# Performance work log

Measured on AMD Instinct MI355X. Metric: run time of the kernel, lower is better.

The kernel has to match this reference:

```python
import jax, jax.numpy as jnp
import numpy as np

B, S, D_IN, D_OUT = 4, 2048, 1024, 1024

def setup_inputs() -> dict:
    key = jax.random.key(0)
    k1, k2, k3, k4, k5, k6 = jax.random.split(key, 6)
    return {
        "inputs_for_keys": jax.random.normal(k1, (B, S, D_IN), dtype=jnp.float32),
        "inputs_for_values": jax.random.normal(k2, (B, S, D_IN), dtype=jnp.float32),
        "inputs_for_queries": jax.random.normal(k3, (B, S, D_IN), dtype=jnp.float32),
        "WK": jax.random.truncated_normal(k4, -2.0, 2.0, (D_IN, D_OUT), dtype=jnp.float32) * 0.1,
        "WV": jax.random.truncated_normal(k5, -2.0, 2.0, (D_IN, D_OUT), dtype=jnp.float32) * 0.1,
        "WQ": jax.random.truncated_normal(k6, -2.0, 2.0, (D_IN, D_OUT), dtype=jnp.float32) * 0.1,
    }

def reference(inputs_for_keys, inputs_for_values, inputs_for_queries, WK, WV, WQ):
    # projections: [B,S,D_in] @ [D_in,D_out] -> [B,S,D_out]
    K = jnp.einsum('bsd,de->bse', inputs_for_keys, WK)
    V = jnp.einsum('bsd,de->bse', inputs_for_values, WV)
    Q = jnp.einsum('bsd,de->bse', inputs_for_queries, WQ)
    # scores: [B,S,S]. NOTE: original TF code scales by sqrt(K.shape[1]) = sqrt(seq_len),
    # not sqrt(head_dim) — reproduce that faithfully.
    scale = jnp.sqrt(jnp.float32(K.shape[1]))
    scores = jnp.einsum('bqe,bke->bqk', Q, K) / scale
    attn = jax.nn.softmax(scores, axis=-1)
    return jnp.einsum('bqk,bke->bqe', attn, V)
```

## Files before the change

### kernel.cpp

```cpp
#include <hip/hip_runtime.h>
#include <hip/hip_bf16.h>


typedef __attribute__((ext_vector_type(4))) float    f32x4;
typedef __attribute__((ext_vector_type(8))) _Float16 f16x8;
typedef __attribute__((ext_vector_type(4))) _Float16 f16x4;

constexpr size_t MiB = 1u << 20;
constexpr size_t MK  = (size_t)8192 * 1024;
constexpr size_t WSZ = (size_t)1024 * 1024;

__device__ __forceinline__ void gload_lds16(const void* g, void* l) {
  __builtin_amdgcn_global_load_lds(
      (const __attribute__((address_space(1))) unsigned int*)g,
      (__attribute__((address_space(3))) unsigned int*)l, 16, 0, 0);
}

#define MFMA16(a, b, c) __builtin_amdgcn_mfma_f32_16x16x32_f16(a, b, c, 0, 0, 0)

__device__ __forceinline__ void swz_block(int& bx, int& by, int& bz) {
  unsigned gx = gridDim.x, gy = gridDim.y;
  unsigned flat = blockIdx.x + gx * (blockIdx.y + gy * blockIdx.z);
  unsigned total = gx * gy * gridDim.z;
  unsigned cpx = total >> 3;
  unsigned s = (flat & 7) * cpx + (flat >> 3);
  bx = s % gx; s /= gx; by = s % gy; bz = s / gy;
}

__global__ __launch_bounds__(256) void prep(
    const float* __restrict__ x0, const float* __restrict__ x1,
    const float* __restrict__ x2, _Float16* __restrict__ XF,
    const float* __restrict__ w0, const float* __restrict__ w1,
    const float* __restrict__ w2, _Float16* __restrict__ WT)
{
  const unsigned id = blockIdx.x;
  if (id < 24576) {
    const int z = id >> 13;
    const unsigned blk = id & 8191;
    const float* x = z == 0 ? x0 : (z == 1 ? x1 : x2);
    size_t i = ((size_t)blk * 256 + threadIdx.x) * 4;
    float4 v = *(const float4*)(x + i);
    f16x4 h = {(_Float16)v.x, (_Float16)v.y, (_Float16)v.z, (_Float16)v.w};
    *(f16x4*)(XF + (size_t)z * MK + i) = h;
  } else {
    const unsigned rem = id - 24576;
    const int z = rem >> 10;
    const unsigned blk = rem & 1023;
    const float* W = z == 0 ? w0 : (z == 1 ? w1 : w2);
    _Float16* o = WT + (size_t)z * WSZ;
    __shared__ float tile[32][33];
    const int bx = (blk & 31) * 32;
    const int by = (blk >> 5) * 32;
    const int tx = threadIdx.x & 31, ty = threadIdx.x >> 5;
    #pragma unroll
    for (int r = 0; r < 32; r += 8)
      tile[ty + r][tx] = W[(size_t)(by + ty + r) * 1024 + bx + tx];
    __syncthreads();
    #pragma unroll
    for (int r = 0; r < 32; r += 8)
      o[(size_t)(bx + ty + r) * 1024 + by + tx] = (_Float16)tile[tx][ty + r];
  }
}

template <int MODE>
__global__ __launch_bounds__(512, 4) void gemmO(
    const _Float16* __restrict__ At, size_t sAz, int lda,
    const _Float16* __restrict__ Bt, size_t sBz, int ldb,
    void* __restrict__ Cv, size_t sCz, int ldc,
    int K, float scale)
{
  extern __shared__ char lds[];
  int bx, by, bz;
  swz_block(bx, by, bz);
  const _Float16* A = At + (size_t)bz * sAz;
  const _Float16* B = Bt + (size_t)bz * sBz;

  const int gm0 = by * 256, gn0 = bx * 128;
  const int tid = threadIdx.x;
  const int lane = tid & 63, wave = tid >> 6;
  const int wm = (wave >> 1) * 64;
  const int wn = (wave & 1) * 64;
  const int fr = lane & 15, fq = lane >> 4;
  const int nkt = K >> 5;

  const int clog = ((tid & 3) ^ ((tid >> 3) & 3)) * 8;
  const _Float16* srcA = A + (size_t)(gm0 + (tid >> 2)) * lda + clog;
  const _Float16* srcB = B + (size_t)(gn0 + (tid >> 2)) * ldb + clog;
  char* const dst0 = lds + tid * 16;

  auto STG = [&](int tile) {
    const int off = tile * 32;
    char* d = dst0 + (tile % 3) * 24576;
    gload_lds16(srcA + off,                     d);
    gload_lds16(srcA + off + (size_t)128 * lda, d + 8192);
    gload_lds16(srcB + off,                     d + 16384);
  };

  const int pc  = (fq ^ ((fr >> 1) & 3)) * 16;
  const int arb = (wm + fr) * 64 + pc;
  const int brb = 16384 + (wn + fr) * 64 + pc;

  f32x4 acc[4][4] = {};
  f16x8 af[4], bfr[4];

  STG(0);
  if (nkt > 1) {
    STG(1);
    asm volatile("s_waitcnt vmcnt(3)" ::: "memory");
  } else {
    asm volatile("s_waitcnt vmcnt(0)" ::: "memory");
  }
  __builtin_amdgcn_s_barrier();
  __builtin_amdgcn_sched_barrier(0);

  for (int t = 0; t < nkt; ++t) {
    const char* buf = lds + (t % 3) * 24576;
    const bool st2 = (t + 2) < nkt;

    if (st2) STG(t + 2);

    #pragma unroll
    for (int mi = 0; mi < 4; ++mi)
      af[mi] = *(const f16x8*)(buf + arb + mi * 1024);
    #pragma unroll
    for (int ni = 0; ni < 4; ++ni)
      bfr[ni] = *(const f16x8*)(buf + brb + ni * 1024);

    __builtin_amdgcn_s_setprio(1);
    #pragma unroll
    for (int mi = 0; mi < 4; ++mi)
      #pragma unroll
      for (int ni = 0; ni < 4; ++ni)
        acc[mi][ni] = MFMA16(af[mi], bfr[ni], acc[mi][ni]);
    __builtin_amdgcn_s_setprio(0);

    if (st2)               asm volatile("s_waitcnt vmcnt(3)" ::: "memory");
    else if (t + 1 < nkt)  asm volatile("s_waitcnt vmcnt(0)" ::: "memory");
    __builtin_amdgcn_s_barrier();
    __builtin_amdgcn_sched_barrier(0);
  }

  const int erow = gm0 + wm + fq * 4;
  const int ecol = gn0 + wn + fr;
  #pragma unroll
  for (int m = 0; m < 4; ++m)
    #pragma unroll
    for (int n = 0; n < 4; ++n) {
      size_t base = (size_t)(erow + m * 16) * ldc + (ecol + n * 16);
      #pragma unroll
      for (int r = 0; r < 4; ++r) {
        float v = acc[m][n][r];
        size_t idx = base + (size_t)r * ldc;
        if constexpr (MODE == 0)
          ((float*)Cv + (size_t)bz * sCz)[idx] = v * scale;
        else if constexpr (MODE == 1)
          ((_Float16*)Cv + (size_t)bz * sCz)[idx] = (_Float16)v;
        else
          ((_Float16*)Cv + (size_t)bz * sCz)[idx] = (_Float16)(v * scale);
      }
    }
}

__global__ __launch_bounds__(256) void softmax_rows(
    const _Float16* __restrict__ S, _Float16* __restrict__ P)
{
  const int w = threadIdx.x >> 6, lane = threadIdx.x & 63;
  const size_t row = (size_t)blockIdx.x * 4 + w;
  const _Float16* sr = S + row * 2048;

  f16x8 v[4];
  #pragma unroll
  for (int c = 0; c < 4; ++c)
    v[c] = *(const f16x8*)(sr + c * 512 + lane * 8);

  float m = -1e30f;
  #pragma unroll
  for (int c = 0; c < 4; ++c)
    #pragma unroll
    for (int j = 0; j < 8; ++j) m = fmaxf(m, (float)v[c][j]);
  #pragma unroll
  for (int o = 32; o >= 1; o >>= 1) m = fmaxf(m, __shfl_xor(m, o));

  float e[4][8];
  float s = 0.f;
  #pragma unroll
  for (int c = 0; c < 4; ++c)
    #pragma unroll
    for (int j = 0; j < 8; ++j) {
      e[c][j] = __expf((float)v[c][j] - m);
      s += e[c][j];
    }
  #pragma unroll
  for (int o = 32; o >= 1; o >>= 1) s += __shfl_xor(s, o);

  const float inv = 1.0f / s;
  _Float16* pr = P + row * 2048;
  #pragma unroll
  for (int c = 0; c < 4; ++c) {
    f16x8 p;
    #pragma unroll
    for (int j = 0; j < 8; ++j) p[j] = (_Float16)(e[c][j] * inv);
    *(f16x8*)(pr + c * 512 + lane * 8) = p;
  }
}

extern "C" void kernel_launch(void* const* d_in, const int* in_sizes, int n_in,
                              void* d_out, int out_size, void* d_ws, size_t ws_size,
                              hipStream_t stream)
{
  const float* Xk = (const float*)d_in[0];
  const float* Xv = (const float*)d_in[1];
  const float* Xq = (const float*)d_in[2];
  const float* WK = (const float*)d_in[3];
  const float* WV = (const float*)d_in[4];
  const float* WQ = (const float*)d_in[5];
  float* out = (float*)d_out;
  char* ws = (char*)d_ws;

  _Float16* XF   = (_Float16*)(ws);
  _Float16* WT   = (_Float16*)(ws + 48 * MiB);
  _Float16* PROJ = (_Float16*)(ws + 54 * MiB);
  _Float16* VTf  = (_Float16*)(ws + 86 * MiB);
  _Float16* SC   = (_Float16*)(ws + 102 * MiB);
  _Float16* P    = (_Float16*)(ws);

  _Float16* Kp = PROJ;
  _Float16* Qp = PROJ + MK;

  auto* f1 = gemmO<1>;
  auto* f2 = gemmO<2>;
  auto* f0 = gemmO<0>;
  (void)hipFuncSetAttribute((const void*)f1, hipFuncAttributeMaxDynamicSharedMemorySize, 73728);
  (void)hipFuncSetAttribute((const void*)f2, hipFuncAttributeMaxDynamicSharedMemorySize, 73728);
  (void)hipFuncSetAttribute((const void*)f0, hipFuncAttributeMaxDynamicSharedMemorySize, 73728);

  prep<<<dim3(27648), 256, 0, stream>>>(Xk, Xv, Xq, XF, WK, WV, WQ, WT);
  gemmO<1><<<dim3(8, 32, 2), 512, 73728, stream>>>(
      XF, 2 * MK, 1024, WT, 2 * WSZ, 1024,
      PROJ, MK, 1024, 1024, 1.0f);
  gemmO<1><<<dim3(64, 4, 1), 512, 73728, stream>>>(
      WT + WSZ, 0, 1024, XF + MK, 0, 1024,
      VTf, 0, 8192, 1024, 1.0f);
  gemmO<2><<<dim3(16, 8, 4), 512, 73728, stream>>>(
      Qp, (size_t)2048 * 1024, 1024, Kp, (size_t)2048 * 1024, 1024,
      SC, (size_t)2048 * 2048, 2048, 1024, 0.022097086912079608f);
  softmax_rows<<<dim3(2048), 256, 0, stream>>>(SC, P);
  gemmO<0><<<dim3(8, 8, 4), 512, 73728, stream>>>(
      P, (size_t)2048 * 2048, 2048, VTf, 2048, 8192,
      out, (size_t)2048 * 1024, 1024, 2048, 1.0f);
}
```

Measured before the change: 195.3 us.

## Add 256x256 8-wave phased GEMM for K/Q projection and QK^T scores

Measured after the change: 183.0 us. -6.3%, faster.

```diff
diff --git a/kernel.cpp b/kernel.cpp
--- a/kernel.cpp
+++ b/kernel.cpp
@@ -34,16 +34,20 @@
     const float* __restrict__ w2, _Float16* __restrict__ WT)
 {
   const unsigned id = blockIdx.x;
-  if (id < 24576) {
-    const int z = id >> 13;
-    const unsigned blk = id & 8191;
-    const float* x = z == 0 ? x0 : (z == 1 ? x1 : x2);
-    size_t i = ((size_t)blk * 256 + threadIdx.x) * 4;
-    float4 v = *(const float4*)(x + i);
-    f16x4 h = {(_Float16)v.x, (_Float16)v.y, (_Float16)v.z, (_Float16)v.w};
-    *(f16x4*)(XF + (size_t)z * MK + i) = h;
+  if (id < 6144) {
+    const int z = id >> 11;
+    const unsigned blk = id & 2047;
+    const float* x = (z == 0 ? x0 : (z == 1 ? x1 : x2)) + (size_t)blk * 4096;
+    _Float16* o = XF + (size_t)z * MK + (size_t)blk * 4096;
+    #pragma unroll
+    for (int j = 0; j < 4; ++j) {
+      size_t i = (size_t)j * 1024 + threadIdx.x * 4;
+      float4 v = *(const float4*)(x + i);
+      f16x4 h = {(_Float16)v.x, (_Float16)v.y, (_Float16)v.z, (_Float16)v.w};
+      *(f16x4*)(o + i) = h;
+    }
   } else {
-    const unsigned rem = id - 24576;
+    const unsigned rem = id - 6144;
     const int z = rem >> 10;
     const unsigned blk = rem & 1023;
     const float* W = z == 0 ? w0 : (z == 1 ? w1 : w2);
@@ -60,6 +64,167 @@
     for (int r = 0; r < 32; r += 8)
       o[(size_t)(bx + ty + r) * 1024 + by + tx] = (_Float16)tile[tx][ty + r];
   }
+}
+
+template <int MODE>
+__global__ __launch_bounds__(512, 2) void gemm8p(
+    const _Float16* __restrict__ At, size_t sA,
+    const _Float16* __restrict__ Bt, size_t sB,
+    void* __restrict__ Cv, size_t sCz,
+    int N, int K, float scale)
+{
+  extern __shared__ char lds[];
+  int bx, by, bz;
+  swz_block(bx, by, bz);
+  const _Float16* A = At + (size_t)bz * sA;
+  const _Float16* B = Bt + (size_t)bz * sB;
+
+  const int gm0 = by * 256, gn0 = bx * 256;
+  const int tid = threadIdx.x;
+  const int lane = tid & 63, wave = tid >> 6;
+  const int wm = (wave >> 2) * 128;
+  const int wn = (wave & 3) * 64;
+  const int fr = lane & 15, fq = lane >> 4;
+  const int nkt = K >> 6;
+
+  const int clog = ((tid & 7) ^ ((tid >> 3) & 7)) * 8;
+  const _Float16* srcA = A + (size_t)(gm0 + (tid >> 3)) * K + clog;
+  const _Float16* srcB = B + (size_t)(gn0 + (tid >> 3)) * K + clog;
+  char* const dst0 = lds + tid * 16;
+
+  auto SH = [&](int tile, int h) {
+    const _Float16* s = (h < 2 ? srcA : srcB) + (size_t)((h & 1) * 128) * K
+                        + tile * 64;
+    char* d = dst0 + (tile & 1) * 65536 + h * 16384;
+    gload_lds16(s, d);
+    gload_lds16(s + (size_t)64 * K, d + 8192);
+  };
+
+  const int axor = fr & 7;
+  const int pc0 = (fq ^ axor) * 16;
+  const int pc1 = ((4 + fq) ^ axor) * 16;
+  const int arb = (wm + fr) * 128;
+  const int brb = 32768 + (wn + fr) * 128;
+
+  f32x4 acc[8][4] = {};
+  f16x8 af[4][2], b0[2][2], b1[2][2];
+
+  SH(0, 0); SH(0, 1); SH(0, 2); SH(0, 3);
+  if (nkt > 1) {
+    SH(1, 0);
+    asm volatile("s_waitcnt vmcnt(2)" ::: "memory");
+  } else {
+    asm volatile("s_waitcnt vmcnt(0)" ::: "memory");
+  }
+  __builtin_amdgcn_s_barrier();
+  __builtin_amdgcn_sched_barrier(0);
+
+#define PHASE_MID                                          \
+  __builtin_amdgcn_s_barrier();                            \
+  asm volatile("s_waitcnt lgkmcnt(0)" ::: "memory");       \
+  __builtin_amdgcn_sched_barrier(0);                       \
+  __builtin_amdgcn_s_setprio(1);
+#define PHASE_END                                          \
+  __builtin_amdgcn_s_setprio(0);                           \
+  __builtin_amdgcn_sched_barrier(0);                       \
+  __builtin_amdgcn_s_barrier();
+
+  for (int t = 0; t < nkt; ++t) {
+    const char* buf = lds + (t & 1) * 65536;
+    const bool st1 = (t + 1) < nkt;
+
+    #pragma unroll
+    for (int mi = 0; mi < 4; ++mi) {
+      af[mi][0] = *(const f16x8*)(buf + arb + mi * 2048 + pc0);
+      af[mi][1] = *(const f16x8*)(buf + arb + mi * 2048 + pc1);
+    }
+    #pragma unroll
+    for (int ni = 0; ni < 2; ++ni) {
+      b0[ni][0] = *(const f16x8*)(buf + brb + ni * 2048 + pc0);
+      b0[ni][1] = *(const f16x8*)(buf + brb + ni * 2048 + pc1);
+    }
+    if (st1) SH(t + 1, 1);
+    PHASE_MID
+    #pragma unroll
+    for (int mi = 0; mi < 4; ++mi)
+      #pragma unroll
+      for (int ni = 0; ni < 2; ++ni)
+        #pragma unroll
+        for (int kk = 0; kk < 2; ++kk)
+          acc[mi][ni] = MFMA16(af[mi][kk], b0[ni][kk], acc[mi][ni]);
+    PHASE_END
+
+    #pragma unroll
+    for (int ni = 0; ni < 2; ++ni) {
+      b1[ni][0] = *(const f16x8*)(buf + brb + (ni + 2) * 2048 + pc0);
+      b1[ni][1] = *(const f16x8*)(buf + brb + (ni + 2) * 2048 + pc1);
+    }
+    if (st1) SH(t + 1, 2);
+    PHASE_MID
+    #pragma unroll
+    for (int mi = 0; mi < 4; ++mi)
+      #pragma unroll
+      for (int ni = 0; ni < 2; ++ni)
+        #pragma unroll
+        for (int kk = 0; kk < 2; ++kk)
+          acc[mi][ni + 2] = MFMA16(af[mi][kk], b1[ni][kk], acc[mi][ni + 2]);
+    PHASE_END
+
+    #pragma unroll
+    for (int mi = 0; mi < 4; ++mi) {
+      af[mi][0] = *(const f16x8*)(buf + arb + (mi + 4) * 2048 + pc0);
+      af[mi][1] = *(const f16x8*)(buf + arb + (mi + 4) * 2048 + pc1);
+    }
+    if (st1) SH(t + 1, 3);
+    PHASE_MID
+    #pragma unroll
+    for (int mi = 0; mi < 4; ++mi)
+      #pragma unroll
+      for (int ni = 0; ni < 2; ++ni)
+        #pragma unroll
+        for (int kk = 0; kk < 2; ++kk)
+          acc[mi + 4][ni] = MFMA16(af[mi][kk], b0[ni][kk], acc[mi + 4][ni]);
+    PHASE_END
+
+    const bool st2 = (t + 2) < nkt;
+    if (st2) SH(t + 2, 0);
+    __builtin_amdgcn_s_barrier();
+    __builtin_amdgcn_s_setprio(1);
+    #pragma unroll
+    for (int mi = 0; mi < 4; ++mi)
+      #pragma unroll
+      for (int ni = 0; ni < 2; ++ni)
+        #pragma unroll
+        for (int kk = 0; kk < 2; ++kk)
+          acc[mi + 4][ni + 2] = MFMA16(af[mi][kk], b1[ni][kk], acc[mi + 4][ni + 2]);
+    __builtin_amdgcn_s_setprio(0);
+    __builtin_amdgcn_sched_barrier(0);
+    if (st2) asm volatile("s_waitcnt vmcnt(2)" ::: "memory");
+    else     asm volatile("s_waitcnt vmcnt(0)" ::: "memory");
+    __builtin_amdgcn_s_barrier();
+  }
+#undef PHASE_MID
+#undef PHASE_END
+
+  const int erow = gm0 + wm + fq * 4;
+  const int ecol = gn0 + wn + fr;
+  #pragma unroll
+  for (int m = 0; m < 8; ++m)
+    #pragma unroll
+    for (int n = 0; n < 4; ++n) {
+      size_t base = (size_t)(erow + m * 16) * N + (ecol + n * 16);
+      #pragma unroll
+      for (int r = 0; r < 4; ++r) {
+        float v = acc[m][n][r];
+        if constexpr (MODE == 0)
+          ((float*)Cv + (size_t)bz * sCz)[base + (size_t)r * N] = v * scale;
+        else if constexpr (MODE == 1)
+          ((_Float16*)Cv + (size_t)bz * sCz)[base + (size_t)r * N] = (_Float16)v;
+        else
+          ((_Float16*)Cv + (size_t)bz * sCz)[base + (size_t)r * N] =
+              (_Float16)(v * scale);
+      }
+    }
 }
 
 template <int MODE>
@@ -227,22 +392,23 @@
   _Float16* Kp = PROJ;
   _Float16* Qp = PROJ + MK;
 
+  auto* g1 = gemm8p<1>;
+  auto* g2 = gemm8p<2>;
   auto* f1 = gemmO<1>;
-  auto* f2 = gemmO<2>;
   auto* f0 = gemmO<0>;
+  (void)hipFuncSetAttribute((const void*)g1, hipFuncAttributeMaxDynamicSharedMemorySize, 131072);
+  (void)hipFuncSetAttribute((const void*)g2, hipFuncAttributeMaxDynamicSharedMemorySize, 131072);
   (void)hipFuncSetAttribute((const void*)f1, hipFuncAttributeMaxDynamicSharedMemorySize, 73728);
-  (void)hipFuncSetAttribute((const void*)f2, hipFuncAttributeMaxDynamicSharedMemorySize, 73728);
   (void)hipFuncSetAttribute((const void*)f0, hipFuncAttributeMaxDynamicSharedMemorySize, 73728);
 
-  prep<<<dim3(27648), 256, 0, stream>>>(Xk, Xv, Xq, XF, WK, WV, WQ, WT);
-  gemmO<1><<<dim3(8, 32, 2), 512, 73728, stream>>>(
-      XF, 2 * MK, 1024, WT, 2 * WSZ, 1024,
-      PROJ, MK, 1024, 1024, 1.0f);
+  prep<<<dim3(9216), 256, 0, stream>>>(Xk, Xv, Xq, XF, WK, WV, WQ, WT);
+  gemm8p<1><<<dim3(4, 32, 2), 512, 131072, stream>>>(
+      XF, 2 * MK, WT, 2 * WSZ, PROJ, MK, 1024, 1024, 1.0f);
   gemmO<1><<<dim3(64, 4, 1), 512, 73728, stream>>>(
       WT + WSZ, 0, 1024, XF + MK, 0, 1024,
       VTf, 0, 8192, 1024, 1.0f);
-  gemmO<2><<<dim3(16, 8, 4), 512, 73728, stream>>>(
-      Qp, (size_t)2048 * 1024, 1024, Kp, (size_t)2048 * 1024, 1024,
+  gemm8p<2><<<dim3(8, 8, 4), 512, 131072, stream>>>(
+      Qp, (size_t)2048 * 1024, Kp, (size_t)2048 * 1024,
       SC, (size_t)2048 * 2048, 2048, 1024, 0.022097086912079608f);
   softmax_rows<<<dim3(2048), 256, 0, stream>>>(SC, P);
   gemmO<0><<<dim3(8, 8, 4), 512, 73728, stream>>>(
```
